# Kernel optimization log

Measured on AMD Instinct MI355X. Metric: run time of the kernel, lower is better.

Reference implementation:

```python
import jax, jax.numpy as jnp
import numpy as np

B, N, C = 8, 8192, 64
P, K = 2048, 16
C_IN = 2 * C + 6   # 134: concat(diff, center) of (feat ++ xyz)
H1, H2 = 64, 128
EPS = 1e-5


def setup_inputs() -> dict:
    key = jax.random.key(0)
    ks = jax.random.split(key, 16)
    inp = {
        "xyz": jax.random.normal(ks[0], (B, N, 3), dtype=jnp.float32),
        "feat": jax.random.normal(ks[1], (B, C, N), dtype=jnp.float32),
        # SharedMLP layer 1: 1x1 conv + BN(eval) + ReLU
        "W1": jax.random.normal(ks[2], (H1, C_IN), dtype=jnp.float32) * (1.0 / np.sqrt(C_IN)),
        "b1": jnp.zeros((H1,), dtype=jnp.float32),
        "g1": jax.random.uniform(ks[3], (H1,), minval=0.5, maxval=1.5, dtype=jnp.float32),
        "be1": jax.random.normal(ks[4], (H1,), dtype=jnp.float32) * 0.1,
        "m1": jax.random.normal(ks[5], (H1,), dtype=jnp.float32) * 0.1,
        "v1": jax.random.uniform(ks[6], (H1,), minval=0.5, maxval=1.5, dtype=jnp.float32),
        # SharedMLP layer 2
        "W2": jax.random.normal(ks[7], (H2, H1), dtype=jnp.float32) * (1.0 / np.sqrt(H1)),
        "b2": jnp.zeros((H2,), dtype=jnp.float32),
        "g2": jax.random.uniform(ks[8], (H2,), minval=0.5, maxval=1.5, dtype=jnp.float32),
        "be2": jax.random.normal(ks[9], (H2,), dtype=jnp.float32) * 0.1,
        "m2": jax.random.normal(ks[10], (H2,), dtype=jnp.float32) * 0.1,
        "v2": jax.random.uniform(ks[11], (H2,), minval=0.5, maxval=1.5, dtype=jnp.float32),
        "npoints": P,
    }
    return inp


def _mlp_layer(x, W, b, g, be, m, v):
    # x: [b,p,k,cin] -> 1x1 conv (einsum) + eval-mode BN + ReLU
    y = jnp.einsum("bpkc,oc->bpko", x, W) + b
    y = g * (y - m) * jax.lax.rsqrt(v + EPS) + be
    return jax.nn.relu(y)


def reference(xyz, feat, W1, b1, g1, be1, m1, v1, W2, b2, g2, be2, m2, v2, npoints):
    p = npoints
    # Range sampling: take first p points
    new_xyz = xyz[:, :p]                       # [b,p,3]
    feat_t = jnp.swapaxes(feat, 1, 2)          # [b,n,c]
    feat_x = jnp.concatenate([feat_t, xyz], axis=-1)   # [b,n,c+3] (use_xyz)
    new_feat_x = feat_x[:, :p]                 # [b,p,c+3]
    # KNN via squared euclidean distance, expanded form to avoid [b,p,n,3]
    sq_q = jnp.sum(new_xyz * new_xyz, axis=-1)           # [b,p]
    sq_r = jnp.sum(xyz * xyz, axis=-1)                   # [b,n]
    dots = jnp.einsum("bpd,bnd->bpn", new_xyz, xyz)      # [b,p,n]
    d2 = sq_q[:, :, None] + sq_r[:, None, :] - 2.0 * dots
    _, idx = jax.lax.top_k(-d2, K)             # [b,p,k] nearest (ascending dist)
    # Gather neighbor features: [b,p,k,c+3]
    knn_feat = jax.vmap(lambda f, i: f[i])(feat_x, idx)
    tiled = jnp.broadcast_to(new_feat_x[:, :, None, :], knn_feat.shape)
    edge = jnp.concatenate([knn_feat - tiled, tiled], axis=-1)  # [b,p,k,2c+6]
    h = _mlp_layer(edge, W1, b1, g1, be1, m1, v1)
    h = _mlp_layer(h, W2, b2, g2, be2, m2, v2)              # [b,p,k,H2]
    new_feat = jnp.swapaxes(jnp.max(h, axis=2), 1, 2)       # [b,H2,p]
    sample_idx = jnp.broadcast_to(jnp.arange(p, dtype=jnp.int32), (xyz.shape[0], p))
    return new_xyz, new_feat, sample_idx
```

## Files before the change

### kernel.cpp

```cpp
#include <hip/hip_runtime.h>
#include <hip/hip_bf16.h>

#define BB 8
#define NN 8192
#define CC 64
#define PP 2048
#define KK 16
#define H1 64
#define H2 128
#define K1PAD 160
#define K2PAD 72

typedef float  f32x4 __attribute__((ext_vector_type(4)));
typedef short  s16x8 __attribute__((ext_vector_type(8)));

#define OFF_FXT   0u
#define OFF_PTS4  17825792u
#define OFF_KNN   19922944u
#define OFF_W1P   20971520u
#define OFF_W2P   20992000u
#define OFF_C1    21010432u
#define OFF_C2    21010688u

#define FLTMAX 3.402823466e+38f

static __device__ __forceinline__ unsigned short bf16b(float v) {
    __hip_bfloat16 h = __float2bfloat16(v);
    return *reinterpret_cast<unsigned short*>(&h);
}
static __device__ __forceinline__ unsigned pk2(float a, float b) {
    return ((unsigned)bf16b(b) << 16) | (unsigned)bf16b(a);
}
static __device__ __forceinline__ unsigned dpk(unsigned v, unsigned t) {
    float v0 = __uint_as_float(v << 16), v1 = __uint_as_float(v & 0xffff0000u);
    float t0 = __uint_as_float(t << 16), t1 = __uint_as_float(t & 0xffff0000u);
    return pk2(v0 - t0, v1 - t1);
}
static __device__ __forceinline__ uint4 dpk4(uint4 v, uint4 t) {
    return make_uint4(dpk(v.x, t.x), dpk(v.y, t.y), dpk(v.z, t.z), dpk(v.w, t.w));
}
#define LDS_FENCE() asm volatile("s_waitcnt lgkmcnt(0)" ::: "memory")

__global__ __launch_bounds__(512) void k1_prep(const float* __restrict__ xyz,
                                               const float* __restrict__ feat,
                                               unsigned* __restrict__ fxtb,
                                               float4* __restrict__ pts4,
                                               float* __restrict__ out0,
                                               float* __restrict__ out2) {
    __shared__ float tile[72][65];
    int b  = blockIdx.x >> 7;
    int n0 = (blockIdx.x & 127) * 64;
    int tx = threadIdx.x & 63, ty = threadIdx.x >> 6;
    for (int c = ty; c < 72; c += 8) {
        float v;
        if (c < 64)       v = feat[((size_t)b * 64 + c) * NN + n0 + tx];
        else if (c < 67)  v = xyz[((size_t)b * NN + n0 + tx) * 3 + (c - 64)];
        else              v = 0.f;
        tile[c][tx] = v;
    }
    __syncthreads();
    size_t base = ((size_t)b * NN + n0) * 36;
    for (int e = threadIdx.x; e < 64 * 36; e += 512) {
        int nl = e / 36, c = e - nl * 36;
        fxtb[base + e] = pk2(tile[2 * c][nl], tile[2 * c + 1][nl]);
    }
    if (threadIdx.x < 64) {
        int n = n0 + threadIdx.x;
        float x = tile[64][threadIdx.x], y = tile[65][threadIdx.x], z = tile[66][threadIdx.x];
        pts4[(size_t)b * NN + n] = make_float4(x, y, z, x * x + y * y + z * z);
        if (n0 < PP) out2[b * PP + n] = (float)n;
    }
    if (n0 < PP) {
        for (int e = threadIdx.x; e < 64 * 3; e += 512) {
            int nl = e / 3, d = e - nl * 3;
            out0[((size_t)b * PP + n0 + nl) * 3 + d] = tile[64 + d][nl];
        }
    }
}

__global__ __launch_bounds__(1024, 2) void k2_knn(const float4* __restrict__ pts4,
                                                  int* __restrict__ knn,
                                                  const float* __restrict__ W1, const float* __restrict__ b1,
                                                  const float* __restrict__ g1, const float* __restrict__ be1,
                                                  const float* __restrict__ m1, const float* __restrict__ v1,
                                                  const float* __restrict__ W2, const float* __restrict__ b2,
                                                  const float* __restrict__ g2, const float* __restrict__ be2,
                                                  const float* __restrict__ m2, const float* __restrict__ v2,
                                                  unsigned short* __restrict__ w1p,
                                                  unsigned short* __restrict__ w2p,
                                                  float* __restrict__ c1, float* __restrict__ c2) {
    __shared__ float4 stage[8192];
    __shared__ float2 scratch[16][2][64];
    int lane = threadIdx.x & 63;
    int wv   = threadIdx.x >> 6;
    int b    = blockIdx.x >> 5;
    int q0   = (blockIdx.x & 31) * 64 + wv * 4;
    size_t pb = (size_t)b * NN;

    float4 qc = make_float4(0.f, 0.f, 0.f, 0.f);
    if (lane < 4) qc = pts4[pb + q0 + lane];
    float qx2 = -2.f * qc.x, qy2 = -2.f * qc.y, qz2 = -2.f * qc.z;
    float bx[4], by[4], bz[4];
#pragma unroll
    for (int q = 0; q < 4; ++q) {
        bx[q] = __shfl(qx2, q); by[q] = __shfl(qy2, q); bz[q] = __shfl(qz2, q);
    }

#pragma unroll
    for (int i = 0; i < 8; ++i) {
        int p = i * 1024 + threadIdx.x;
        float4 v = pts4[pb + p];
        int r = p >> 6, c = p & 63;
        stage[(r << 6) | ((c + (r >> 1)) & 63)] = v;
    }

    if (threadIdx.x < 77) {
        int i = blockIdx.x * 77 + threadIdx.x;
        if (i < 64 * K1PAD) {
            int n = i / K1PAD, c = i - n * K1PAD;
            float s = g1[n] * rsqrtf(v1[n] + 1e-5f);
            float val = 0.f;
            if (c < 67)                  val = W1[n * 134 + c] * s;
            else if (c >= 72 && c < 139) val = W1[n * 134 + (c - 5)] * s;
            w1p[i] = bf16b(val);
        } else if (i < 19456) {
            int j = i - 10240;
            int o = j / K2PAD, k = j - o * K2PAD;
            float s = g2[o] * rsqrtf(v2[o] + 1e-5f);
            w2p[j] = bf16b((k < 64) ? W2[o * 64 + k] * s : 0.f);
        } else if (i < 19520) {
            int l = i - 19456;
            float s = g1[l] * rsqrtf(v1[l] + 1e-5f);
            c1[l] = s * (b1[l] - m1[l]) + be1[l];
        } else if (i < 19648) {
            int p = i - 19520;
            float s = g2[p] * rsqrtf(v2[p] + 1e-5f);
            c2[p] = s * (b2[p] - m2[p]) + be2[p];
        }
    }
    __syncthreads();

    float m[4];
#pragma unroll
    for (int q = 0; q < 4; ++q) m[q] = FLTMAX;
#pragma unroll
    for (int rr = 0; rr < 2; ++rr) {
        int rowbase = (2 * lane + rr) << 6;
#pragma unroll
        for (int j8 = 0; j8 < 8; ++j8) {
            float4 cc[8];
#pragma unroll
            for (int i = 0; i < 8; ++i)
                cc[i] = stage[rowbase | ((j8 * 8 + i + lane) & 63)];
#pragma unroll
            for (int q = 0; q < 4; ++q) {
                float x = bx[q], y = by[q], z = bz[q];
#pragma unroll
                for (int i = 0; i < 8; i += 2) {
                    float e0 = fmaf(z, cc[i].z, fmaf(y, cc[i].y, fmaf(x, cc[i].x, cc[i].w)));
                    float e1 = fmaf(z, cc[i+1].z, fmaf(y, cc[i+1].y, fmaf(x, cc[i+1].x, cc[i+1].w)));
                    m[q] = fminf(fminf(m[q], e0), e1);
                }
            }
        }
    }

    float sv0 = m[0], sv1 = m[1], sv2 = m[2], sv3 = m[3];
#pragma unroll
    for (int k = 2; k <= 64; k <<= 1) {
#pragma unroll
        for (int j = k >> 1; j > 0; j >>= 1) {
            bool keepMin = (((lane & k) == 0) == ((lane & j) == 0));
            float p0 = __shfl_xor(sv0, j, 64);
            float p1 = __shfl_xor(sv1, j, 64);
            float p2 = __shfl_xor(sv2, j, 64);
            float p3 = __shfl_xor(sv3, j, 64);
            sv0 = keepMin ? fminf(sv0, p0) : fmaxf(sv0, p0);
            sv1 = keepMin ? fminf(sv1, p1) : fmaxf(sv1, p1);
            sv2 = keepMin ? fminf(sv2, p2) : fmaxf(sv2, p2);
            sv3 = keepMin ? fminf(sv3, p3) : fmaxf(sv3, p3);
        }
    }
    float T[4];
    T[0] = __shfl(sv0, 15, 64); T[1] = __shfl(sv1, 15, 64);
    T[2] = __shfl(sv2, 15, 64); T[3] = __shfl(sv3, 15, 64);

    unsigned long long below = (lane == 63) ? 0x7FFFFFFFFFFFFFFFull
                                            : ((1ull << lane) - 1ull);
#pragma unroll
    for (int pr = 0; pr < 4; pr += 2) {
        int Ms[2];
#pragma unroll
        for (int u = 0; u < 2; ++u) {
            int q = pr + u;
            float x = bx[q], y = by[q], z = bz[q], tq = T[q];
            unsigned long long rm = __ballot(m[q] <= tq);
            int cnt = 0;
            while (rm) {
                int sl = __ffsll((long long)rm) - 1; rm &= rm - 1;
                int phys = (lane + sl) & 63;
                float4 c0 = stage[((2 * sl) << 6) | phys];
                float4 c1v_ = stage[((2 * sl + 1) << 6) | phys];
                float e0 = fmaf(z, c0.z, fmaf(y, c0.y, fmaf(x, c0.x, c0.w)));
                float e1 = fmaf(z, c1v_.z, fmaf(y, c1v_.y, fmaf(x, c1v_.x, c1v_.w)));
                unsigned long long b0 = __ballot(e0 <= tq);
                if (e0 <= tq) {
                    int pos = cnt + __popcll(b0 & below);
                    if (pos < 64)
                        scratch[wv][u][pos] = make_float2(e0, __int_as_float(sl * 128 + lane));
                }
                cnt += __popcll(b0);
                unsigned long long b1 = __ballot(e1 <= tq);
                if (e1 <= tq) {
                    int pos = cnt + __popcll(b1 & below);
                    if (pos < 64)
                        scratch[wv][u][pos] = make_float2(e1, __int_as_float(sl * 128 + 64 + lane));
                }
                cnt += __popcll(b1);
            }
            Ms[u] = min(cnt, 64);
        }
        LDS_FENCE();
#pragma unroll
        for (int u = 0; u < 2; ++u) {
            int M = Ms[u];
            float2 own = scratch[wv][u][lane];
            float di = own.x; int ni = __float_as_int(own.y);
            int rank = 0;
            const float2* buf = &scratch[wv][u][0];
#pragma unroll 4
            for (int j = 0; j < M; ++j) {
                float2 e = buf[j];
                int nj = __float_as_int(e.y);
                rank += (e.x < di || (e.x == di && nj < ni)) ? 1 : 0;
            }
            if (lane < M && rank < 16)
                knn[((size_t)(b * PP + q0 + pr + u)) * KK + rank] = ni;
        }
        LDS_FENCE();
    }
}

__global__ __launch_bounds__(256, 2) void k3_mlp(const unsigned* __restrict__ fxtb,
                                                 const int* __restrict__ knn,
                                                 const unsigned short* __restrict__ w1p,
                                                 const unsigned short* __restrict__ w2p,
                                                 const float* __restrict__ c1,
                                                 const float* __restrict__ c2,
                                                 float* __restrict__ out1) {
    __shared__ __align__(16) char smem[4 * 5632];
    __shared__ float otile[16][132];
    __shared__ __align__(16) unsigned short w1lds[64 * 168];
    int lane = threadIdx.x & 63;
    int wv   = threadIdx.x >> 6;
    int b    = blockIdx.x & 7;
    int qg   = blockIdx.x >> 3;
    int qbase = qg * 16;
    char* seg = smem + wv * 5632;
    uint4* sh_tc = (uint4*)(seg + 5120);
    unsigned short* h1l = (unsigned short*)(seg);
    const uint4* fx4 = (const uint4*)fxtb;

    int col = lane & 15, quad = lane >> 4;
    int r = lane >> 2, s = lane & 3;

    {
        const unsigned* src = (const unsigned*)w1p;
        unsigned* dst = (unsigned*)w1lds;
        for (int t = threadIdx.x; t < 5120; t += 256) {
            int row = t / 80, c = t - row * 80;
            dst[row * 84 + c] = src[t];
        }
    }

    s16x8 w2f[2][8];
#pragma unroll
    for (int ks = 0; ks < 2; ++ks)
#pragma unroll
        for (int nt = 0; nt < 8; ++nt)
            w2f[ks][nt] = *(const s16x8*)(w2p + (nt * 16 + col) * K2PAD + ks * 32 + quad * 8);
    float c1v[4], c2v[8];
#pragma unroll
    for (int nt = 0; nt < 4; ++nt) c1v[nt] = c1[nt * 16 + col];
#pragma unroll
    for (int nt = 0; nt < 8; ++nt) c2v[nt] = c2[nt * 16 + col];

    int idxAll = knn[((size_t)(b * PP + qbase + wv * 4)) * KK + lane];

    __syncthreads();

    uint4 cc[2][3];
    uint4 tv[2];

#define PREFETCH(buf, qi_) {                                                  \
        int q_ = qbase + wv * 4 + (qi_);                                      \
        if (lane < 9) tv[buf] = fx4[((size_t)b * NN + q_) * 9 + lane];        \
        int nidx_ = __shfl(idxAll, (qi_) * 16 + r, 64);                       \
        const uint4* rowp_ = fx4 + ((size_t)b * NN + nidx_) * 9;              \
        cc[buf][0] = rowp_[s];                                                \
        cc[buf][1] = rowp_[4 + s];                                            \
        if (s == 0) cc[buf][2] = rowp_[8]; }

    PREFETCH(0, 0);

#pragma unroll
    for (int qi = 0; qi < 4; ++qi) {
        int cur = qi & 1, nxt = cur ^ 1;
        if (lane < 9) sh_tc[lane] = tv[cur];
        LDS_FENCE();
        char* erow = seg + r * 320;
        {
            uint4 v = cc[cur][0], t = sh_tc[s];
            *(uint4*)(erow + s * 16) = dpk4(v, t);
            v = cc[cur][1]; t = sh_tc[4 + s];
            *(uint4*)(erow + (4 + s) * 16) = dpk4(v, t);
            if (s == 0) {
                v = cc[cur][2]; t = sh_tc[8];
                *(uint4*)(erow + 128) = dpk4(v, t);
            }
        }
        for (int j = s; j < 9; j += 4)
            *(uint4*)(erow + (9 + j) * 16) = sh_tc[j];
        if (s < 2)
            *(uint4*)(erow + (18 + s) * 16) = make_uint4(0u, 0u, 0u, 0u);
        if (qi < 3) PREFETCH(nxt, qi + 1);
        LDS_FENCE();
        f32x4 acc1[4];
#pragma unroll
        for (int nt = 0; nt < 4; ++nt) acc1[nt] = (f32x4){0.f, 0.f, 0.f, 0.f};
#pragma unroll
        for (int ks = 0; ks < 5; ++ks) {
            s16x8 a = *(const s16x8*)(seg + col * 320 + ks * 64 + quad * 16);
#pragma unroll
            for (int nt = 0; nt < 4; ++nt) {
                s16x8 bf = *(const s16x8*)(w1lds + (nt * 16 + col) * 168 + ks * 32 + quad * 8);
                acc1[nt] = __builtin_amdgcn_mfma_f32_16x16x32_bf16(a, bf, acc1[nt], 0, 0, 0);
            }
        }
#pragma unroll
        for (int nt = 0; nt < 4; ++nt) {
#pragma unroll
            for (int rr = 0; rr < 4; ++rr) {
                float y = fmaxf(acc1[nt][rr] + c1v[nt], 0.f);
                h1l[(quad * 4 + rr) * K2PAD + nt * 16 + col] = bf16b(y);
            }
        }
        LDS_FENCE();
        f32x4 acc2[8];
#pragma unroll
        for (int nt = 0; nt < 8; ++nt) acc2[nt] = (f32x4){0.f, 0.f, 0.f, 0.f};
#pragma unroll
        for (int ks = 0; ks < 2; ++ks) {
            s16x8 a = *(const s16x8*)(seg + col * 144 + ks * 64 + quad * 16);
#pragma unroll
            for (int nt = 0; nt < 8; ++nt)
                acc2[nt] = __builtin_amdgcn_mfma_f32_16x16x32_bf16(a, w2f[ks][nt], acc2[nt], 0, 0, 0);
        }
#pragma unroll
        for (int nt = 0; nt < 8; ++nt) {
            float m0 = fmaxf(fmaxf(acc2[nt][0], acc2[nt][1]), fmaxf(acc2[nt][2], acc2[nt][3]));
            m0 = m0 + c2v[nt];
            m0 = fmaxf(m0, 0.f);
            m0 = fmaxf(m0, __shfl_xor(m0, 16, 64));
            m0 = fmaxf(m0, __shfl_xor(m0, 32, 64));
            if (quad == 0)
                otile[wv * 4 + qi][nt * 16 + col] = m0;
        }
        LDS_FENCE();
    }
    __syncthreads();
    for (int i = threadIdx.x; i < H2 * 16; i += 256) {
        int ch = i >> 4, q = i & 15;
        out1[((size_t)(b * H2 + ch)) * PP + qbase + q] = otile[q][ch];
    }
#undef PREFETCH
}

extern "C" void kernel_launch(void* const* d_in, const int* in_sizes, int n_in,
                              void* d_out, int out_size, void* d_ws, size_t ws_size,
                              hipStream_t stream) {
    const float* xyz  = (const float*)d_in[0];
    const float* feat = (const float*)d_in[1];
    const float* W1   = (const float*)d_in[2];
    const float* b1   = (const float*)d_in[3];
    const float* g1   = (const float*)d_in[4];
    const float* be1  = (const float*)d_in[5];
    const float* m1   = (const float*)d_in[6];
    const float* v1   = (const float*)d_in[7];
    const float* W2   = (const float*)d_in[8];
    const float* b2   = (const float*)d_in[9];
    const float* g2   = (const float*)d_in[10];
    const float* be2  = (const float*)d_in[11];
    const float* m2   = (const float*)d_in[12];
    const float* v2   = (const float*)d_in[13];

    char* ws = (char*)d_ws;
    unsigned*       fxtb = (unsigned*)(ws + OFF_FXT);
    float4*         pts4 = (float4*)(ws + OFF_PTS4);
    int*            knn  = (int*)(ws + OFF_KNN);
    unsigned short* w1p  = (unsigned short*)(ws + OFF_W1P);
    unsigned short* w2p  = (unsigned short*)(ws + OFF_W2P);
    float*          c1   = (float*)(ws + OFF_C1);
    float*          c2   = (float*)(ws + OFF_C2);

    float* out0 = (float*)d_out;
    float* out1 = out0 + (size_t)BB * PP * 3;
    float* out2 = out1 + (size_t)BB * H2 * PP;

    hipLaunchKernelGGL(k1_prep, dim3(1024), dim3(512), 0, stream,
                       xyz, feat, fxtb, pts4, out0, out2);
    hipLaunchKernelGGL(k2_knn, dim3(256), dim3(1024), 0, stream, pts4, knn,
                       W1, b1, g1, be1, m1, v1, W2, b2, g2, be2, m2, v2,
                       w1p, w2p, c1, c2);
    hipLaunchKernelGGL(k3_mlp, dim3(1024), dim3(256), 0, stream,
                       fxtb, knn, w1p, w2p, c1, c2, out1);
}
```

Baseline: 166.1 us.

## Factor layer-1 conv into neighbor and center terms, feed MFMA directly from registers

Rewrites the first MLP layer using W1·[x_j−x_i, x_i] = W1a·x_j + (W1b−W1a)·x_i, so the per-center term is computed once per query with MFMA and used as the accumulator seed. Neighbor rows are loaded straight into MFMA A-fragments in registers instead of building the edge matrix in LDS, and W1 fragments are held in registers instead of being staged in LDS. This removes the bf16 difference packing, the LDS staging, the fences and the W1 LDS copy, and cuts the layer-1 K dimension from 160 to 96. In exchange it raises register pressure and changes rounding, since the center term is now folded into the weights in bf16 and x_j is no longer differenced before conversion.

```diff
diff --git a/kernel.cpp b/kernel.cpp
--- a/kernel.cpp
+++ b/kernel.cpp
@@ -8,7 +8,6 @@
 #define KK 16
 #define H1 64
 #define H2 128
-#define K1PAD 160
 #define K2PAD 72
 
 typedef float  f32x4 __attribute__((ext_vector_type(4)));
@@ -18,9 +17,9 @@
 #define OFF_PTS4  17825792u
 #define OFF_KNN   19922944u
 #define OFF_W1P   20971520u
-#define OFF_W2P   20992000u
-#define OFF_C1    21010432u
-#define OFF_C2    21010688u
+#define OFF_W2P   20996096u
+#define OFF_C1    21014528u
+#define OFF_C2    21014784u
 
 #define FLTMAX 3.402823466e+38f
 
@@ -31,13 +30,8 @@
 static __device__ __forceinline__ unsigned pk2(float a, float b) {
     return ((unsigned)bf16b(b) << 16) | (unsigned)bf16b(a);
 }
-static __device__ __forceinline__ unsigned dpk(unsigned v, unsigned t) {
-    float v0 = __uint_as_float(v << 16), v1 = __uint_as_float(v & 0xffff0000u);
-    float t0 = __uint_as_float(t << 16), t1 = __uint_as_float(t & 0xffff0000u);
-    return pk2(v0 - t0, v1 - t1);
-}
-static __device__ __forceinline__ uint4 dpk4(uint4 v, uint4 t) {
-    return make_uint4(dpk(v.x, t.x), dpk(v.y, t.y), dpk(v.z, t.z), dpk(v.w, t.w));
+static __device__ __forceinline__ s16x8 as8(uint4 v) {
+    union { uint4 u; s16x8 s; } x; x.u = v; return x.s;
 }
 #define LDS_FENCE() asm volatile("s_waitcnt lgkmcnt(0)" ::: "memory")
 
@@ -114,26 +108,29 @@
         stage[(r << 6) | ((c + (r >> 1)) & 63)] = v;
     }
 
-    if (threadIdx.x < 77) {
-        int i = blockIdx.x * 77 + threadIdx.x;
-        if (i < 64 * K1PAD) {
-            int n = i / K1PAD, c = i - n * K1PAD;
+    if (threadIdx.x < 85) {
+        int i = blockIdx.x * 85 + threadIdx.x;
+        if (i < 6144) {
+            int n = i / 96, c = i - n * 96;
             float s = g1[n] * rsqrtf(v1[n] + 1e-5f);
-            float val = 0.f;
-            if (c < 67)                  val = W1[n * 134 + c] * s;
-            else if (c >= 72 && c < 139) val = W1[n * 134 + (c - 5)] * s;
-            w1p[i] = bf16b(val);
-        } else if (i < 19456) {
-            int j = i - 10240;
-            int o = j / K2PAD, k = j - o * K2PAD;
+            w1p[n * 192 + c] = bf16b((c < 67) ? W1[n * 134 + c] * s : 0.f);
+        } else if (i < 12288) {
+            int j = i - 6144;
+            int n = j / 96, c = j - n * 96;
+            float s = g1[n] * rsqrtf(v1[n] + 1e-5f);
+            w1p[n * 192 + 96 + c] =
+                bf16b((c < 67) ? (W1[n * 134 + 67 + c] - W1[n * 134 + c]) * s : 0.f);
+        } else if (i < 21504) {
+            int j = i - 12288;
+            int o = j / 72, k = j - o * 72;
             float s = g2[o] * rsqrtf(v2[o] + 1e-5f);
             w2p[j] = bf16b((k < 64) ? W2[o * 64 + k] * s : 0.f);
-        } else if (i < 19520) {
-            int l = i - 19456;
+        } else if (i < 21568) {
+            int l = i - 21504;
             float s = g1[l] * rsqrtf(v1[l] + 1e-5f);
             c1[l] = s * (b1[l] - m1[l]) + be1[l];
-        } else if (i < 19648) {
-            int p = i - 19520;
+        } else if (i < 21696) {
+            int p = i - 21568;
             float s = g2[p] * rsqrtf(v2[p] + 1e-5f);
             c2[p] = s * (b2[p] - m2[p]) + be2[p];
         }
@@ -248,119 +245,113 @@
                                                  const float* __restrict__ c1,
                                                  const float* __restrict__ c2,
                                                  float* __restrict__ out1) {
-    __shared__ __align__(16) char smem[4 * 5632];
+    __shared__ __align__(16) unsigned short h1l[4][16 * K2PAD];
     __shared__ float otile[16][132];
-    __shared__ __align__(16) unsigned short w1lds[64 * 168];
     int lane = threadIdx.x & 63;
     int wv   = threadIdx.x >> 6;
     int b    = blockIdx.x & 7;
     int qg   = blockIdx.x >> 3;
     int qbase = qg * 16;
-    char* seg = smem + wv * 5632;
-    uint4* sh_tc = (uint4*)(seg + 5120);
-    unsigned short* h1l = (unsigned short*)(seg);
+    int col = lane & 15, quad = lane >> 4;
     const uint4* fx4 = (const uint4*)fxtb;
-
-    int col = lane & 15, quad = lane >> 4;
-    int r = lane >> 2, s = lane & 3;
-
+    size_t rowb = (size_t)b * NN;
+
+    f32x4 accq[4];
+#pragma unroll
+    for (int nt = 0; nt < 4; ++nt) accq[nt] = (f32x4){0.f, 0.f, 0.f, 0.f};
     {
-        const unsigned* src = (const unsigned*)w1p;
-        unsigned* dst = (unsigned*)w1lds;
-        for (int t = threadIdx.x; t < 5120; t += 256) {
-            int row = t / 80, c = t - row * 80;
-            dst[row * 84 + c] = src[t];
-        }
-    }
-
-    s16x8 w2f[2][8];
+        const uint4* rp = fx4 + (rowb + qbase + wv * 4 + col) * 9;
+        uint4 qf0 = rp[quad];
+        uint4 qf1 = rp[4 + quad];
+        uint4 qf2 = rp[8];
+        if (quad != 0) qf2 = make_uint4(0u, 0u, 0u, 0u);
+        uint4 qf[3] = {qf0, qf1, qf2};
+#pragma unroll
+        for (int ks = 0; ks < 3; ++ks) {
+            s16x8 a = as8(qf[ks]);
+#pragma unroll
+            for (int nt = 0; nt < 4; ++nt) {
+                s16x8 bfr = *(const s16x8*)(w1p + (nt * 16 + col) * 192 + 96 + ks * 32 + quad * 8);
+                accq[nt] = __builtin_amdgcn_mfma_f32_16x16x32_bf16(a, bfr, accq[nt], 0, 0, 0);
+            }
+        }
+    }
+    float qc[4][4];
+    {
+        float c1v[4];
+#pragma unroll
+        for (int nt = 0; nt < 4; ++nt) c1v[nt] = c1[nt * 16 + col];
+#pragma unroll
+        for (int qi = 0; qi < 4; ++qi)
+#pragma unroll
+            for (int nt = 0; nt < 4; ++nt)
+                qc[qi][nt] = __shfl(accq[nt][qi], col, 64) + c1v[nt];
+    }
+
+    s16x8 w1f[3][4], w2f[2][8];
+#pragma unroll
+    for (int ks = 0; ks < 3; ++ks)
+#pragma unroll
+        for (int nt = 0; nt < 4; ++nt)
+            w1f[ks][nt] = *(const s16x8*)(w1p + (nt * 16 + col) * 192 + ks * 32 + quad * 8);
 #pragma unroll
     for (int ks = 0; ks < 2; ++ks)
 #pragma unroll
         for (int nt = 0; nt < 8; ++nt)
             w2f[ks][nt] = *(const s16x8*)(w2p + (nt * 16 + col) * K2PAD + ks * 32 + quad * 8);
-    float c1v[4], c2v[8];
-#pragma unroll
-    for (int nt = 0; nt < 4; ++nt) c1v[nt] = c1[nt * 16 + col];
+    float c2v[8];
 #pragma unroll
     for (int nt = 0; nt < 8; ++nt) c2v[nt] = c2[nt * 16 + col];
 
     int idxAll = knn[((size_t)(b * PP + qbase + wv * 4)) * KK + lane];
-
-    __syncthreads();
-
-    uint4 cc[2][3];
-    uint4 tv[2];
-
-#define PREFETCH(buf, qi_) {                                                  \
-        int q_ = qbase + wv * 4 + (qi_);                                      \
-        if (lane < 9) tv[buf] = fx4[((size_t)b * NN + q_) * 9 + lane];        \
-        int nidx_ = __shfl(idxAll, (qi_) * 16 + r, 64);                       \
-        const uint4* rowp_ = fx4 + ((size_t)b * NN + nidx_) * 9;              \
-        cc[buf][0] = rowp_[s];                                                \
-        cc[buf][1] = rowp_[4 + s];                                            \
-        if (s == 0) cc[buf][2] = rowp_[8]; }
-
-    PREFETCH(0, 0);
+    unsigned short* h1w = &h1l[wv][0];
+
+    uint4 af[2][3];
+#define PREF(buf, qi_) {                                                      \
+        int nidx_ = __shfl(idxAll, (qi_) * 16 + col, 64);                     \
+        const uint4* rp_ = fx4 + (rowb + nidx_) * 9;                          \
+        af[buf][0] = rp_[quad];                                               \
+        af[buf][1] = rp_[4 + quad];                                           \
+        uint4 f2_ = rp_[8];                                                   \
+        af[buf][2] = (quad == 0) ? f2_ : make_uint4(0u, 0u, 0u, 0u); }
+
+    PREF(0, 0);
 
 #pragma unroll
     for (int qi = 0; qi < 4; ++qi) {
-        int cur = qi & 1, nxt = cur ^ 1;
-        if (lane < 9) sh_tc[lane] = tv[cur];
-        LDS_FENCE();
-        char* erow = seg + r * 320;
-        {
-            uint4 v = cc[cur][0], t = sh_tc[s];
-            *(uint4*)(erow + s * 16) = dpk4(v, t);
-            v = cc[cur][1]; t = sh_tc[4 + s];
-            *(uint4*)(erow + (4 + s) * 16) = dpk4(v, t);
-            if (s == 0) {
-                v = cc[cur][2]; t = sh_tc[8];
-                *(uint4*)(erow + 128) = dpk4(v, t);
-            }
-        }
-        for (int j = s; j < 9; j += 4)
-            *(uint4*)(erow + (9 + j) * 16) = sh_tc[j];
-        if (s < 2)
-            *(uint4*)(erow + (18 + s) * 16) = make_uint4(0u, 0u, 0u, 0u);
-        if (qi < 3) PREFETCH(nxt, qi + 1);
-        LDS_FENCE();
+        const int cur = qi & 1;
         f32x4 acc1[4];
 #pragma unroll
-        for (int nt = 0; nt < 4; ++nt) acc1[nt] = (f32x4){0.f, 0.f, 0.f, 0.f};
-#pragma unroll
-        for (int ks = 0; ks < 5; ++ks) {
-            s16x8 a = *(const s16x8*)(seg + col * 320 + ks * 64 + quad * 16);
-#pragma unroll
-            for (int nt = 0; nt < 4; ++nt) {
-                s16x8 bf = *(const s16x8*)(w1lds + (nt * 16 + col) * 168 + ks * 32 + quad * 8);
-                acc1[nt] = __builtin_amdgcn_mfma_f32_16x16x32_bf16(a, bf, acc1[nt], 0, 0, 0);
-            }
-        }
-#pragma unroll
-        for (int nt = 0; nt < 4; ++nt) {
-#pragma unroll
-            for (int rr = 0; rr < 4; ++rr) {
-                float y = fmaxf(acc1[nt][rr] + c1v[nt], 0.f);
-                h1l[(quad * 4 + rr) * K2PAD + nt * 16 + col] = bf16b(y);
-            }
-        }
+        for (int nt = 0; nt < 4; ++nt)
+            acc1[nt] = (f32x4){qc[qi][nt], qc[qi][nt], qc[qi][nt], qc[qi][nt]};
+#pragma unroll
+        for (int ks = 0; ks < 3; ++ks) {
+            s16x8 a = as8(af[cur][ks]);
+#pragma unroll
+            for (int nt = 0; nt < 4; ++nt)
+                acc1[nt] = __builtin_amdgcn_mfma_f32_16x16x32_bf16(a, w1f[ks][nt], acc1[nt], 0, 0, 0);
+        }
+        if (qi < 3) PREF(cur ^ 1, qi + 1);
+#pragma unroll
+        for (int nt = 0; nt < 4; ++nt)
+#pragma unroll
+            for (int rr = 0; rr < 4; ++rr)
+                h1w[(quad * 4 + rr) * K2PAD + nt * 16 + col] = bf16b(fmaxf(acc1[nt][rr], 0.f));
         LDS_FENCE();
         f32x4 acc2[8];
 #pragma unroll
         for (int nt = 0; nt < 8; ++nt) acc2[nt] = (f32x4){0.f, 0.f, 0.f, 0.f};
 #pragma unroll
         for (int ks = 0; ks < 2; ++ks) {
-            s16x8 a = *(const s16x8*)(seg + col * 144 + ks * 64 + quad * 16);
+            s16x8 a2 = *(const s16x8*)(h1w + col * K2PAD + ks * 32 + quad * 8);
 #pragma unroll
             for (int nt = 0; nt < 8; ++nt)
-                acc2[nt] = __builtin_amdgcn_mfma_f32_16x16x32_bf16(a, w2f[ks][nt], acc2[nt], 0, 0, 0);
+                acc2[nt] = __builtin_amdgcn_mfma_f32_16x16x32_bf16(a2, w2f[ks][nt], acc2[nt], 0, 0, 0);
         }
 #pragma unroll
         for (int nt = 0; nt < 8; ++nt) {
             float m0 = fmaxf(fmaxf(acc2[nt][0], acc2[nt][1]), fmaxf(acc2[nt][2], acc2[nt][3]));
-            m0 = m0 + c2v[nt];
-            m0 = fmaxf(m0, 0.f);
+            m0 = fmaxf(m0 + c2v[nt], 0.f);
             m0 = fmaxf(m0, __shfl_xor(m0, 16, 64));
             m0 = fmaxf(m0, __shfl_xor(m0, 32, 64));
             if (quad == 0)
@@ -373,7 +364,7 @@
         int ch = i >> 4, q = i & 15;
         out1[((size_t)(b * H2 + ch)) * PP + qbase + q] = otile[q][ch];
     }
-#undef PREFETCH
+#undef PREF
 }
 
 extern "C" void kernel_launch(void* const* d_in, const int* in_sizes, int n_in,
```

Result: faster. 161.6 us (-2.7%).
